# Kernel optimization log

Hardware: AMD Instinct MI355X
Metric: run time of the kernel (lower is better)

## Reference

```python
import jax, jax.numpy as jnp
import numpy as np
import math

D_MODEL = 1024
NHEAD = 16
HEAD_DIM = D_MODEL // NHEAD
ROPE_BASE = 10000.0


def _rope(x):
    # x: [B, H, S, Dh]; rotate per the RoPE class (half-split variant)
    d = x.shape[-1]
    half = d // 2
    seq_len = x.shape[2]
    theta = 1.0 / (ROPE_BASE ** (jnp.arange(0, d, 2, dtype=jnp.float32) / d))  # [d/2]
    ang = jnp.arange(seq_len, dtype=jnp.float32)[:, None] * theta[None, :]      # [S, d/2]
    ang2 = jnp.concatenate([ang, ang], axis=-1)                                 # [S, d]
    cos_ = jnp.cos(ang2)[None, None, :, :]
    sin_ = jnp.sin(ang2)[None, None, :, :]
    neg_half = jnp.concatenate([-x[..., half:], x[..., :half]], axis=-1)
    return x * cos_ + neg_half * sin_


def setup_inputs() -> dict:
    key = jax.random.key(0)
    ks = jax.random.split(key, 10)
    B, S, D = 4, 2048, D_MODEL
    scale = 1.0 / math.sqrt(D)
    x = jax.random.normal(ks[0], (B, S, D), dtype=jnp.float32)
    Wq = jax.random.normal(ks[1], (D, D), dtype=jnp.float32) * scale
    bq = jnp.zeros((D,), dtype=jnp.float32)
    Wk = jax.random.normal(ks[2], (D, D), dtype=jnp.float32) * scale
    bk = jnp.zeros((D,), dtype=jnp.float32)
    Wv = jax.random.normal(ks[3], (D, D), dtype=jnp.float32) * scale
    bv = jnp.zeros((D,), dtype=jnp.float32)
    Wo = jax.random.normal(ks[4], (D, D), dtype=jnp.float32) * scale
    bo = jnp.zeros((D,), dtype=jnp.float32)
    # causal mask: mask==1 means masked (upper triangle)
    mask = jnp.triu(jnp.ones((S, S), dtype=jnp.int32), k=1)[None, None, :, :]
    return {"x": x, "Wq": Wq, "bq": bq, "Wk": Wk, "bk": bk,
            "Wv": Wv, "bv": bv, "Wo": Wo, "bo": bo, "mask": mask}


def reference(x, Wq, bq, Wk, bk, Wv, bv, Wo, bo, mask):
    B, S, D = x.shape
    H, Dh = NHEAD, HEAD_DIM

    def proj(W, b):
        y = jnp.einsum('bsd,ed->bse', x, W) + b  # torch Linear: x @ W.T + b
        return y.reshape(B, S, H, Dh).transpose(0, 2, 1, 3)  # [B,H,S,Dh]

    q = _rope(proj(Wq, bq))
    k = _rope(proj(Wk, bk))
    v = proj(Wv, bv)

    a = jnp.einsum('bhqd,bhkd->bhqk', q, k) / math.sqrt(Dh)  # [B,H,S,S]
    a = jnp.where(mask == 1, jnp.float32(-1e9), a)
    a = jax.nn.softmax(a, axis=-1)
    out = jnp.einsum('bhqk,bhkd->bhqd', a, v)                 # [B,H,S,Dh]
    out = out.transpose(0, 2, 1, 3).reshape(B, S, D)
    return jnp.einsum('bsd,ed->bse', out, Wo) + bo
```

## Files before the change

kernel.cpp:

```cpp
#include <hip/hip_runtime.h>
#include <stdint.h>

typedef unsigned short u16;
typedef __bf16 bf16x8 __attribute__((ext_vector_type(8)));
typedef __bf16 bf16x2 __attribute__((ext_vector_type(2)));
typedef float f32x4 __attribute__((ext_vector_type(4)));
typedef float f32x16 __attribute__((ext_vector_type(16)));

#define SEQ    2048
#define NHEAD  16
#define DH     64
#define DMODEL 1024
#define NBH    64

__device__ __forceinline__ u16 cvt1(float f){
  union { __bf16 h; u16 u; } c; c.h = (__bf16)f; return c.u;
}
__device__ __forceinline__ uint32_t cvt2(float a, float b){
  union { bf16x2 v; uint32_t u; } c; c.v = bf16x2{(__bf16)a, (__bf16)b}; return c.u;
}
__device__ __forceinline__ int swz(int row){ return (((row&7)^((row>>3)&7))<<4); }

#if __has_builtin(__builtin_amdgcn_exp2f)
__device__ __forceinline__ float EXP2(float x){ return __builtin_amdgcn_exp2f(x); }
#else
__device__ __forceinline__ float EXP2(float x){ return exp2f(x); }
#endif
__device__ __forceinline__ float max3f(float a, float b, float c){
  float r; asm("v_max3_f32 %0, %1, %2, %3" : "=v"(r) : "v"(a), "v"(b), "v"(c));
  return r;
}

typedef const __attribute__((address_space(1))) uint32_t* gas_t;
typedef __attribute__((address_space(3))) uint32_t* las_t;
__device__ __forceinline__ void async16(const void* g, void* l){
  __builtin_amdgcn_global_load_lds((gas_t)g, (las_t)l, 16, 0, 0);
}

__device__ __forceinline__ void vstore8(char* dst, uint2 a0, uint2 a1,
                                        uint2 b0, uint2 b1, int dc, int vpos){
  uint32_t pk[8];
  pk[0] = __builtin_amdgcn_perm(b0.x, a0.x, 0x05040100u);
  pk[1] = __builtin_amdgcn_perm(b0.x, a0.x, 0x07060302u);
  pk[2] = __builtin_amdgcn_perm(b0.y, a0.y, 0x05040100u);
  pk[3] = __builtin_amdgcn_perm(b0.y, a0.y, 0x07060302u);
  pk[4] = __builtin_amdgcn_perm(b1.x, a1.x, 0x05040100u);
  pk[5] = __builtin_amdgcn_perm(b1.x, a1.x, 0x07060302u);
  pk[6] = __builtin_amdgcn_perm(b1.y, a1.y, 0x05040100u);
  pk[7] = __builtin_amdgcn_perm(b1.y, a1.y, 0x07060302u);
#pragma unroll
  for (int e=0;e<8;e++){
    const int row = dc*8 + e;
    *(uint32_t*)(dst + ((row*128 + vpos*2) ^ swz(row))) = pk[e];
  }
}

__global__ void prep(const float* __restrict__ x,  const float* __restrict__ Wq,
                     const float* __restrict__ Wk, const float* __restrict__ Wv,
                     const float* __restrict__ Wo,
                     u16* __restrict__ xb, u16* __restrict__ wqkv,
                     u16* __restrict__ wob, float* __restrict__ tab)
{
  const int bid = blockIdx.x, tid = threadIdx.x;
  if (bid < 6144){
    const float* src; u16* dst; int lb;
    if      (bid < 4096){ src = x;  dst = xb;              lb = bid; }
    else if (bid < 4608){ src = Wq; dst = wqkv;            lb = bid-4096; }
    else if (bid < 5120){ src = Wk; dst = wqkv + 1048576;  lb = bid-4608; }
    else if (bid < 5632){ src = Wv; dst = wqkv + 2097152;  lb = bid-5120; }
    else                { src = Wo; dst = wob;             lb = bid-5632; }
    const size_t off = (size_t)lb*2048 + tid*8;
    float4 a = *(const float4*)(src+off);
    float4 b = *(const float4*)(src+off+4);
    bf16x8 o = { (__bf16)a.x,(__bf16)a.y,(__bf16)a.z,(__bf16)a.w,
                 (__bf16)b.x,(__bf16)b.y,(__bf16)b.z,(__bf16)b.w };
    *(bf16x8*)(dst+off) = o;
  } else {
    const int t = (bid-6144)*256 + tid;
    const int s = t >> 5, j = t & 31;
    double freq = exp(-(double)(2*j)/64.0*log(10000.0));
    double ang = (double)s*freq;
    tab[s*64 + 2*j]     = (float)cos(ang);
    tab[s*64 + 2*j + 1] = (float)sin(ang);
  }
}

template<int MODE>
__global__ __launch_bounds__(256, 2)
void gemm_bt(const u16* __restrict__ A, const u16* __restrict__ W,
             const float* __restrict__ b0, const float* __restrict__ b1,
             const float* __restrict__ b2, float* __restrict__ fout,
             u16* __restrict__ dq, u16* __restrict__ dk, u16* __restrict__ dv,
             const float* __restrict__ tab)
{
  __shared__ u16 Ab[2][128*32];
  __shared__ u16 Bb[2][128*32];
  const int tid = threadIdx.x;
  const int lane = tid & 63;
  const int w = tid >> 6, wr = w >> 1, wc = w & 1;
  const int m0 = blockIdx.y * 128;
  const int n0 = blockIdx.x * 128;
  const int c0 = lane & 15, g = lane >> 4;

  f32x4 acc[4][4] = {};

  const int sr = tid >> 2;
  const int sc = (tid & 3) * 8;
  const int stoff = sr*32 + sc;
  const u16* ga = A + (size_t)(m0 + sr) * DMODEL + sc;
  const u16* gb = W + (size_t)(n0 + sr) * DMODEL + sc;

#define STAGE_G(buf, kk) do{ \
    async16(ga + (kk),             Ab[buf] + stoff); \
    async16(ga + (kk) + 64*DMODEL, Ab[buf] + stoff + 64*32); \
    async16(gb + (kk),             Bb[buf] + stoff); \
    async16(gb + (kk) + 64*DMODEL, Bb[buf] + stoff + 64*32); \
  }while(0)

  STAGE_G(0, 0);
  __syncthreads();

#pragma unroll 2
  for (int k0 = 0; k0 < DMODEL; k0 += 32) {
    const int cur = (k0 >> 5) & 1;
    if (k0 + 32 < DMODEL) STAGE_G(cur^1, k0 + 32);
    bf16x8 afr[4], bfr[4];
#pragma unroll
    for (int i=0;i<4;i++) afr[i] = *(const bf16x8*)(Ab[cur] + (wr*64 + i*16 + c0)*32 + g*8);
#pragma unroll
    for (int j=0;j<4;j++) bfr[j] = *(const bf16x8*)(Bb[cur] + (wc*64 + j*16 + c0)*32 + g*8);
    __builtin_amdgcn_s_setprio(1);
#pragma unroll
    for (int i=0;i<4;i++)
#pragma unroll
      for (int j=0;j<4;j++)
        acc[i][j] = __builtin_amdgcn_mfma_f32_16x16x32_bf16(afr[i], bfr[j], acc[i][j], 0,0,0);
    __builtin_amdgcn_s_setprio(0);
    __syncthreads();
  }
#undef STAGE_G

  const int nbase = n0 + wc*64;
  const int t = n0 >> 10;
  const float* bias = (MODE==1) ? b0 : (t==0) ? b0 : (t==1) ? b1 : b2;
  float bv4[4];
#pragma unroll
  for (int j=0;j<4;j++) bv4[j] = bias[(nbase & 1023) + j*16 + c0];

  if (MODE == 0) {
    u16* dst = (t==0) ? dq : (t==1) ? dk : dv;
    const float qs = (t==0) ? 0.18033688011f : 1.0f;
    const int h = (nbase >> 6) & (NHEAD-1);
#pragma unroll
    for (int i=0;i<4;i++){
      const int mbase = m0 + wr*64 + i*16 + g*4;
#pragma unroll
      for (int r=0;r<4;r++){
        const int mm = mbase + r;
        const int bb = mm >> 11, s = mm & (SEQ-1);
        const size_t rowbase = (((size_t)(bb*NHEAD + h))*SEQ + s)*DH;
        if (t < 2) {
#pragma unroll
          for (int j2=0;j2<2;j2++){
            const int dh = j2*16 + c0;
            const float xl = acc[i][j2][r]   + bv4[j2];
            const float xh = acc[i][j2+2][r] + bv4[j2+2];
            const float2 cs = *(const float2*)(tab + (size_t)s*64 + dh*2);
            dst[rowbase + dh]      = cvt1((xl*cs.x - xh*cs.y)*qs);
            dst[rowbase + dh + 32] = cvt1((xh*cs.x + xl*cs.y)*qs);
          }
        } else {
#pragma unroll
          for (int j=0;j<4;j++)
            dst[rowbase + j*16 + c0] = cvt1(acc[i][j][r] + bv4[j]);
        }
      }
    }
  } else {
#pragma unroll
    for (int i=0;i<4;i++){
      const int mbase = m0 + wr*64 + i*16 + g*4;
#pragma unroll
      for (int j=0;j<4;j++){
#pragma unroll
        for (int r=0;r<4;r++)
          fout[(size_t)(mbase + r) * DMODEL + nbase + j*16 + c0] = acc[i][j][r] + bv4[j];
      }
    }
  }
}

__global__ __launch_bounds__(256, 2)
void attn_fwd(const u16* __restrict__ Q, const u16* __restrict__ K,
              const u16* __restrict__ V, u16* __restrict__ O)
{
  __shared__ u16 Kb[2][64*64];
  __shared__ u16 Vt[2][64*64];
  const int bh = blockIdx.x;
  const int pair = blockIdx.y;
  const int tid = threadIdx.x, lane = tid & 63, w = tid >> 6;
  const int c31 = lane & 31, hi = lane >> 5;
  const size_t hb = (size_t)bh * SEQ * DH;
  const int b = bh >> 4, h = bh & 15;

  const int boff1 = tid*16;
  const int ksw1  = boff1 ^ swz(boff1 >> 7);
  const int boff2 = boff1 + 4096;
  const int ksw2  = boff2 ^ swz(boff2 >> 7);
  const int rp = tid >> 3, dc = tid & 7;
  const int kv0 = 2*rp;
  const int vpos = (kv0 & 0x33) | ((kv0 & 4) << 1) | ((kv0 & 8) >> 1);

#pragma unroll 1
  for (int half = 0; half < 2; half++){
    const int qt = half ? (15 - pair) : pair;
    const int qrow_base = qt*128 + w*32;
    const int jt_last  = 2*qt + 1;
    const int jt_end_w = 2*qt + (w>>1);
    const int q = qrow_base + c31;

    bf16x8 qf[4];
#pragma unroll
    for (int kc=0;kc<4;kc++)
      qf[kc] = *(const bf16x8*)(Q + hb + (size_t)q*DH + kc*16 + hi*8);

    f32x16 oacc0 = {}, oacc1 = {};
    float mrun = -3.0e38f, lrun = 0.f;

    {
      const char* gk = (const char*)(K + hb);
      async16(gk + ksw1, (char*)Kb[0] + boff1);
      async16(gk + ksw2, (char*)Kb[0] + boff2);
      const u16* gv = V + hb;
      uint2 a0 = *(const uint2*)(gv + (kv0  )*DH + dc*8);
      uint2 a1 = *(const uint2*)(gv + (kv0  )*DH + dc*8 + 4);
      uint2 b0 = *(const uint2*)(gv + (kv0+1)*DH + dc*8);
      uint2 b1 = *(const uint2*)(gv + (kv0+1)*DH + dc*8 + 4);
      vstore8((char*)Vt[0], a0, a1, b0, b1, dc, vpos);
    }
    __syncthreads();

    uint2 pa0, pa1, pb0, pb1;
    for (int jt = 0; jt <= jt_last; jt++){
      const int cur = jt & 1, nxt = cur ^ 1;
      const bool pre = (jt < jt_last);
      if (pre){
        const char* gk = (const char*)(K + hb + (size_t)(jt+1)*64*DH);
        async16(gk + ksw1, (char*)Kb[nxt] + boff1);
        async16(gk + ksw2, (char*)Kb[nxt] + boff2);
        const u16* gv = V + hb + (size_t)(jt+1)*64*DH;
        pa0 = *(const uint2*)(gv + (kv0  )*DH + dc*8);
        pa1 = *(const uint2*)(gv + (kv0  )*DH + dc*8 + 4);
        pb0 = *(const uint2*)(gv + (kv0+1)*DH + dc*8);
        pb1 = *(const uint2*)(gv + (kv0+1)*DH + dc*8 + 4);
      }

      if (jt <= jt_end_w){
        f32x16 sT[2] = {};
#pragma unroll
        for (int kc=0;kc<4;kc++){
          const int col = (kc*16 + hi*8)*2;
          const int r0 = c31, r1 = 32 + c31;
          const bf16x8 kf0 = *(const bf16x8*)((const char*)Kb[cur] + ((r0*128 + col) ^ swz(r0)));
          const bf16x8 kf1 = *(const bf16x8*)((const char*)Kb[cur] + ((r1*128 + col) ^ swz(r1)));
          __builtin_amdgcn_s_setprio(1);
          sT[0] = __builtin_amdgcn_mfma_f32_32x32x16_bf16(kf0, qf[kc], sT[0], 0,0,0);
          sT[1] = __builtin_amdgcn_mfma_f32_32x32x16_bf16(kf1, qf[kc], sT[1], 0,0,0);
          __builtin_amdgcn_s_setprio(0);
        }
        if (jt == jt_end_w){
#pragma unroll
          for (int kvb=0;kvb<2;kvb++)
#pragma unroll
            for (int r=0;r<16;r++){
              const int kv = jt*64 + kvb*32 + (r&3) + 8*(r>>2) + 4*hi;
              sT[kvb][r] = (kv <= q) ? sT[kvb][r] : -3.0e38f;
            }
        }
        float mx0 = -3.0e38f, mx1 = -3.0e38f;
#pragma unroll
        for (int r=0;r<16;r+=2){
          mx0 = max3f(mx0, sT[0][r], sT[0][r+1]);
          mx1 = max3f(mx1, sT[1][r], sT[1][r+1]);
        }
        float mx = fmaxf(mx0, mx1);
        mx = fmaxf(mx, __shfl_xor(mx, 32));
        const bool grow = __any(mx > mrun + 8.0f);
        float corr = 1.0f;
        if (grow){
          const float mnew = fmaxf(mrun, mx);
          corr = EXP2(mrun - mnew);
          mrun = mnew;
        }
        float ls[4] = {0.f, 0.f, 0.f, 0.f};
#pragma unroll
        for (int kvb=0;kvb<2;kvb++)
#pragma unroll
          for (int r=0;r<16;r++){
            const float p = EXP2(sT[kvb][r] - mrun);
            sT[kvb][r] = p;
            ls[r & 3] += p;
          }
        float lsum = (ls[0] + ls[1]) + (ls[2] + ls[3]);
        lsum += __shfl_xor(lsum, 32);
        lrun = lrun*corr + lsum;
        if (grow){
#pragma unroll
          for (int r=0;r<16;r++){ oacc0[r] *= corr; oacc1[r] *= corr; }
        }
#pragma unroll
        for (int kvb=0;kvb<2;kvb++)
#pragma unroll
          for (int s=0;s<2;s++){
            union { bf16x8 v; uint32_t d[4]; } pa;
#pragma unroll
            for (int j=0;j<4;j++)
              pa.d[j] = cvt2(sT[kvb][s*8+2*j], sT[kvb][s*8+2*j+1]);
            const int col = (kvb*32 + s*16 + hi*8)*2;
            const int r0 = c31, r1 = 32 + c31;
            const bf16x8 vf0 = *(const bf16x8*)((const char*)Vt[cur] + ((r0*128 + col) ^ swz(r0)));
            const bf16x8 vf1 = *(const bf16x8*)((const char*)Vt[cur] + ((r1*128 + col) ^ swz(r1)));
            __builtin_amdgcn_s_setprio(1);
            oacc0 = __builtin_amdgcn_mfma_f32_32x32x16_bf16(vf0, pa.v, oacc0, 0,0,0);
            oacc1 = __builtin_amdgcn_mfma_f32_32x32x16_bf16(vf1, pa.v, oacc1, 0,0,0);
            __builtin_amdgcn_s_setprio(0);
          }
      }

      if (pre) vstore8((char*)Vt[nxt], pa0, pa1, pb0, pb1, dc, vpos);
      __syncthreads();
    }

    {
      const float inv = 1.0f / lrun;
      u16* orow = O + ((size_t)b*SEQ + q)*DMODEL + h*DH;
#pragma unroll
      for (int r2=0;r2<8;r2++){
        const int dh0 = 2*(r2&1) + 8*(r2>>1) + 4*hi;
        *(uint32_t*)(orow + dh0)      = cvt2(oacc0[2*r2]*inv, oacc0[2*r2+1]*inv);
        *(uint32_t*)(orow + 32 + dh0) = cvt2(oacc1[2*r2]*inv, oacc1[2*r2+1]*inv);
      }
    }
  }
}

extern "C" void kernel_launch(void* const* d_in, const int* in_sizes, int n_in,
                              void* d_out, int out_size, void* d_ws, size_t ws_size,
                              hipStream_t stream)
{
  const float* x  = (const float*)d_in[0];
  const float* Wq = (const float*)d_in[1];
  const float* bq = (const float*)d_in[2];
  const float* Wk = (const float*)d_in[3];
  const float* bk = (const float*)d_in[4];
  const float* Wv = (const float*)d_in[5];
  const float* bv = (const float*)d_in[6];
  const float* Wo = (const float*)d_in[7];
  const float* bo = (const float*)d_in[8];

  const size_t MB = 1024*1024;
  char* ws = (char*)d_ws;
  u16*  xb   = (u16*)(ws);
  u16*  aw   = (u16*)(ws);
  u16*  vw   = (u16*)(ws + 16*MB);
  u16*  wqkv = (u16*)(ws + 32*MB);
  u16*  wob  = (u16*)(ws + 38*MB);
  float* tab = (float*)(ws + 41*MB);
  u16*  qw = (u16*)d_out;
  u16*  kw = (u16*)d_out + 8*MB;

  prep<<<dim3(6400), dim3(256), 0, stream>>>(x, Wq, Wk, Wv, Wo, xb, wqkv, wob, tab);

  gemm_bt<0><<<dim3(24, 64), dim3(256), 0, stream>>>(xb, wqkv, bq, bk, bv,
                                                     nullptr, qw, kw, vw, tab);

  attn_fwd<<<dim3(64, 8), dim3(256), 0, stream>>>(qw, kw, vw, aw);

  gemm_bt<1><<<dim3(8, 64), dim3(256), 0, stream>>>(aw, wob, bo, nullptr, nullptr,
                                                    (float*)d_out, nullptr, nullptr, nullptr, nullptr);
}
```

Measured before the change: 176.0 us.

## Single-buffer GEMM LDS tiles with XOR swizzle instead of double buffering

Replaces the double-buffered async LDS staging in the projection GEMM with a single buffer that is loaded and consumed within each k-step, bracketed by two barriers. An XOR swizzle is applied to the global source column so that LDS fragment reads avoid bank conflicts. This halves LDS use per block, which may raise occupancy. The cost is that global loads no longer overlap the MFMA work.

Measured after the change: 175.0 us. About the same (-0.5%).

```diff
diff --git a/kernel.cpp b/kernel.cpp
--- a/kernel.cpp
+++ b/kernel.cpp
@@ -93,8 +93,8 @@
              u16* __restrict__ dq, u16* __restrict__ dk, u16* __restrict__ dv,
              const float* __restrict__ tab)
 {
-  __shared__ u16 Ab[2][128*32];
-  __shared__ u16 Bb[2][128*32];
+  __shared__ u16 Ab[128*32];
+  __shared__ u16 Bb[128*32];
   const int tid = threadIdx.x;
   const int lane = tid & 63;
   const int w = tid >> 6, wr = w >> 1, wc = w & 1;
@@ -105,30 +105,30 @@
   f32x4 acc[4][4] = {};
 
   const int sr = tid >> 2;
-  const int sc = (tid & 3) * 8;
-  const int stoff = sr*32 + sc;
-  const u16* ga = A + (size_t)(m0 + sr) * DMODEL + sc;
-  const u16* gb = W + (size_t)(n0 + sr) * DMODEL + sc;
-
-#define STAGE_G(buf, kk) do{ \
-    async16(ga + (kk),             Ab[buf] + stoff); \
-    async16(ga + (kk) + 64*DMODEL, Ab[buf] + stoff + 64*32); \
-    async16(gb + (kk),             Bb[buf] + stoff); \
-    async16(gb + (kk) + 64*DMODEL, Bb[buf] + stoff + 64*32); \
-  }while(0)
-
-  STAGE_G(0, 0);
-  __syncthreads();
-
-#pragma unroll 2
+  const int sc16 = tid & 3;
+  const int stoff = sr*64 + sc16*16;
+  const int gsw = (sc16*16) ^ ((sr & 3) << 4);
+  const char* ga = (const char*)A + (size_t)(m0 + sr)*DMODEL*2 + gsw;
+  const char* gb = (const char*)W + (size_t)(n0 + sr)*DMODEL*2 + gsw;
+
   for (int k0 = 0; k0 < DMODEL; k0 += 32) {
-    const int cur = (k0 >> 5) & 1;
-    if (k0 + 32 < DMODEL) STAGE_G(cur^1, k0 + 32);
+    __syncthreads();
+    async16(ga + 2*k0,              (char*)Ab + stoff);
+    async16(ga + 2*k0 + 128*DMODEL, (char*)Ab + stoff + 4096);
+    async16(gb + 2*k0,              (char*)Bb + stoff);
+    async16(gb + 2*k0 + 128*DMODEL, (char*)Bb + stoff + 4096);
+    __syncthreads();
     bf16x8 afr[4], bfr[4];
 #pragma unroll
-    for (int i=0;i<4;i++) afr[i] = *(const bf16x8*)(Ab[cur] + (wr*64 + i*16 + c0)*32 + g*8);
-#pragma unroll
-    for (int j=0;j<4;j++) bfr[j] = *(const bf16x8*)(Bb[cur] + (wc*64 + j*16 + c0)*32 + g*8);
+    for (int i=0;i<4;i++){
+      const int row = wr*64 + i*16 + c0;
+      afr[i] = *(const bf16x8*)((const char*)Ab + row*64 + ((g*16) ^ ((row&3)<<4)));
+    }
+#pragma unroll
+    for (int j=0;j<4;j++){
+      const int row = wc*64 + j*16 + c0;
+      bfr[j] = *(const bf16x8*)((const char*)Bb + row*64 + ((g*16) ^ ((row&3)<<4)));
+    }
     __builtin_amdgcn_s_setprio(1);
 #pragma unroll
     for (int i=0;i<4;i++)
@@ -136,9 +136,7 @@
       for (int j=0;j<4;j++)
         acc[i][j] = __builtin_amdgcn_mfma_f32_16x16x32_bf16(afr[i], bfr[j], acc[i][j], 0,0,0);
     __builtin_amdgcn_s_setprio(0);
-    __syncthreads();
-  }
-#undef STAGE_G
+  }
 
   const int nbase = n0 + wc*64;
   const int t = n0 >> 10;
```

## Swizzle GEMM LDS tiles and overlap async loads with explicit vmcnt waits

Applied to the files above, without the earlier changes.

Reworks the projection GEMM main loop so the next tile's async global-to-LDS loads stay in flight while the current tile is computed. It waits with a partial vmcnt count and raw s_barrier instead of a full __syncthreads, and peels the final iteration. It also XOR-swizzles the 64-byte LDS rows, by changing the global source addresses, to cut bank conflicts on the fragment reads. The cost is hand-managed wait counts and barriers, which depend on exactly four loads per stage and are fragile.

New measurement: 172.2 us. 1.02x faster.

```diff
diff --git a/kernel.cpp b/kernel.cpp
--- a/kernel.cpp
+++ b/kernel.cpp
@@ -105,40 +105,58 @@
   f32x4 acc[4][4] = {};
 
   const int sr = tid >> 2;
-  const int sc = (tid & 3) * 8;
-  const int stoff = sr*32 + sc;
-  const u16* ga = A + (size_t)(m0 + sr) * DMODEL + sc;
-  const u16* gb = W + (size_t)(n0 + sr) * DMODEL + sc;
+  const int sc16 = tid & 3;
+  const int stoff = sr*64 + sc16*16;
+  const int gsw = (sc16*16) ^ ((sr & 3) << 4);
+  const char* ga = (const char*)A + (size_t)(m0 + sr)*DMODEL*2 + gsw;
+  const char* gb = (const char*)W + (size_t)(n0 + sr)*DMODEL*2 + gsw;
 
 #define STAGE_G(buf, kk) do{ \
-    async16(ga + (kk),             Ab[buf] + stoff); \
-    async16(ga + (kk) + 64*DMODEL, Ab[buf] + stoff + 64*32); \
-    async16(gb + (kk),             Bb[buf] + stoff); \
-    async16(gb + (kk) + 64*DMODEL, Bb[buf] + stoff + 64*32); \
+    async16(ga + 2*(kk),              (char*)Ab[buf] + stoff); \
+    async16(ga + 2*(kk) + 128*DMODEL, (char*)Ab[buf] + stoff + 4096); \
+    async16(gb + 2*(kk),              (char*)Bb[buf] + stoff); \
+    async16(gb + 2*(kk) + 128*DMODEL, (char*)Bb[buf] + stoff + 4096); \
   }while(0)
 
+#define COMPUTE_G(buf) do{ \
+    bf16x8 afr[4], bfr[4]; \
+    _Pragma("unroll") \
+    for (int i=0;i<4;i++){ \
+      const int row = wr*64 + i*16 + c0; \
+      afr[i] = *(const bf16x8*)((const char*)Ab[buf] + row*64 + ((g*16) ^ ((row&3)<<4))); \
+    } \
+    _Pragma("unroll") \
+    for (int j=0;j<4;j++){ \
+      const int row = wc*64 + j*16 + c0; \
+      bfr[j] = *(const bf16x8*)((const char*)Bb[buf] + row*64 + ((g*16) ^ ((row&3)<<4))); \
+    } \
+    __builtin_amdgcn_s_setprio(1); \
+    _Pragma("unroll") \
+    for (int i=0;i<4;i++) \
+      _Pragma("unroll") \
+      for (int j=0;j<4;j++) \
+        acc[i][j] = __builtin_amdgcn_mfma_f32_16x16x32_bf16(afr[i], bfr[j], acc[i][j], 0,0,0); \
+    __builtin_amdgcn_s_setprio(0); \
+  }while(0)
+
   STAGE_G(0, 0);
-  __syncthreads();
-
 #pragma unroll 2
-  for (int k0 = 0; k0 < DMODEL; k0 += 32) {
+  for (int k0 = 0; k0 < DMODEL - 32; k0 += 32) {
     const int cur = (k0 >> 5) & 1;
-    if (k0 + 32 < DMODEL) STAGE_G(cur^1, k0 + 32);
-    bf16x8 afr[4], bfr[4];
-#pragma unroll
-    for (int i=0;i<4;i++) afr[i] = *(const bf16x8*)(Ab[cur] + (wr*64 + i*16 + c0)*32 + g*8);
-#pragma unroll
-    for (int j=0;j<4;j++) bfr[j] = *(const bf16x8*)(Bb[cur] + (wc*64 + j*16 + c0)*32 + g*8);
-    __builtin_amdgcn_s_setprio(1);
-#pragma unroll
-    for (int i=0;i<4;i++)
-#pragma unroll
-      for (int j=0;j<4;j++)
-        acc[i][j] = __builtin_amdgcn_mfma_f32_16x16x32_bf16(afr[i], bfr[j], acc[i][j], 0,0,0);
-    __builtin_amdgcn_s_setprio(0);
-    __syncthreads();
-  }
+    STAGE_G(cur ^ 1, k0 + 32);
+    asm volatile("s_waitcnt vmcnt(4)" ::: "memory");
+    __builtin_amdgcn_s_barrier();
+    __builtin_amdgcn_sched_barrier(0);
+    COMPUTE_G(cur);
+    __builtin_amdgcn_s_barrier();
+    __builtin_amdgcn_sched_barrier(0);
+  }
+  asm volatile("s_waitcnt vmcnt(0)" ::: "memory");
+  __builtin_amdgcn_s_barrier();
+  __builtin_amdgcn_sched_barrier(0);
+  COMPUTE_G(1);
 #undef STAGE_G
+#undef COMPUTE_G
 
   const int nbase = n0 + wc*64;
   const int t = n0 >> 10;
```
